# Performance work log

Hardware: AMD Instinct MI355X
Metric: run time of the kernel (lower is better)

Reference implementation:

```python
import jax, jax.numpy as jnp
import numpy as np

DT = 0.01
T, D_IN, D_STATE = 262144, 64, 128

def setup_inputs() -> dict:
    key = jax.random.key(0)
    k1, k2, k3, k4 = jax.random.split(key, 4)
    U = jax.random.normal(k1, (T, D_IN), dtype=jnp.float32)
    A_log = jax.random.normal(k2, (D_STATE,), dtype=jnp.float32) * 0.1 - 1.0
    B = jax.random.normal(k3, (D_STATE, D_IN), dtype=jnp.float32) * 0.1
    C = jax.random.normal(k4, (D_IN, D_STATE), dtype=jnp.float32) * 0.1
    Dm = jnp.zeros((D_IN, D_IN), dtype=jnp.float32)
    h0 = jnp.zeros((D_STATE,), dtype=jnp.float32)
    return {"U": U, "A_log": A_log, "B": B, "C": C, "D": Dm, "h0": h0}

def reference(U, A_log, B, C, D, h0):
    # Discretized diagonal transition: A_disc = exp(A_log * dt)
    A_d = jnp.exp(A_log * DT)  # (d_state,)
    Bu = U @ B.T               # (T, d_state), precompute all input injections
    Du = U @ D.T               # (T, d_input)

    def step(h, bu):
        h_new = A_d * h + bu
        return h_new, h_new

    h_final, H = jax.lax.scan(step, h0, Bu)  # H: (T, d_state)
    Y = H @ C.T + Du                          # (T, d_input)
    return Y, h_final
```

## Files before the change

### kernel.cpp

```cpp
#include <hip/hip_runtime.h>


#define TT   262144
#define DIN  64
#define DS   128
#define DTC  0.01f
#define L    128
#define NG   (TT / L)
#define SEGL 16
#define NSEG (NG / SEGL)

typedef short  s8v  __attribute__((ext_vector_type(8)));
typedef short  s4v  __attribute__((ext_vector_type(4)));
typedef float  f4v  __attribute__((ext_vector_type(4)));

__device__ __forceinline__ unsigned short f2bf(float f) {
    union { __bf16 h; unsigned short u; } cv;
    cv.h = (__bf16)f;
    return cv.u;
}

__device__ __forceinline__ s8v pack8(float4 a, float4 b) {
    union { unsigned short u[8]; s8v v; } r;
    r.u[0] = f2bf(a.x); r.u[1] = f2bf(a.y); r.u[2] = f2bf(a.z); r.u[3] = f2bf(a.w);
    r.u[4] = f2bf(b.x); r.u[5] = f2bf(b.y); r.u[6] = f2bf(b.z); r.u[7] = f2bf(b.w);
    return r.v;
}

__device__ __forceinline__ s4v pack4(float x, float y, float z, float w) {
    union { unsigned short u[4]; s4v v; } r;
    r.u[0] = f2bf(x); r.u[1] = f2bf(y); r.u[2] = f2bf(z); r.u[3] = f2bf(w);
    return r.v;
}

__device__ __forceinline__ int gidx(int NCO, int rtile, int co, int mf) {
    return (((rtile * NCO + co) << 4) + (mf ^ (co & 15))) << 3;
}

__device__ __forceinline__ s8v ldfrag(const unsigned short* S, int NCO,
                                      int rtile, int kt, int q, int m) {
    return *(const s8v*)&S[gidx(NCO, rtile, kt * 4 + q, m)];
}

__device__ __forceinline__ void stage_U(const float* __restrict__ Ug,
                                        unsigned short* __restrict__ sA,
                                        int tid) {
    #pragma unroll
    for (int p = 0; p < 2; ++p) {
        int u  = tid + p * 512;
        int co = u & 7, m = (u >> 3) & 15, mt = u >> 7;
        const float4* gp = (const float4*)(Ug + (mt * 16 + m) * DIN + co * 8);
        *(s8v*)&sA[gidx(8, mt, co, m)] = pack8(gp[0], gp[1]);
    }
}

__device__ __forceinline__ s8v load_bfrag(const float* __restrict__ M,
                                          int row, int k0, int ld) {
    const float4* p = (const float4*)(M + row * ld + k0);
    return pack8(p[0], p[1]);
}

__global__ __launch_bounds__(512) void ssm_k1(
    const float* __restrict__ U, const float* __restrict__ Alog,
    const float* __restrict__ B, float* __restrict__ agg,
    float* __restrict__ segAgg)
{
    __shared__ __align__(16) unsigned short sA[8192];
    const int g    = blockIdx.x;
    const int tid  = threadIdx.x;
    const int lane = tid & 63;
    const int w    = tid >> 6;
    const int q    = lane >> 4, m = lane & 15;
    const int s    = 16 * w + m;

    stage_U(U + (size_t)g * L * DIN, sA, tid);

    s8v Bf[2];
    #pragma unroll
    for (int ks = 0; ks < 2; ++ks)
        Bf[ks] = load_bfrag(B, s, ks * 32 + q * 8, DIN);

    const float cA = Alog[s] * DTC;
    __syncthreads();

    float ainv = __expf(-cA);
    float a16i = __expf(-16.f * cA);
    float wmt  = __expf(cA * (float)(127 - 4 * q));
    float wsum = 0.f;
    #pragma unroll
    for (int mt = 0; mt < 8; ++mt) {
        f4v acc = (f4v){0.f, 0.f, 0.f, 0.f};
        #pragma unroll
        for (int ks = 0; ks < 2; ++ks)
            acc = __builtin_amdgcn_mfma_f32_16x16x32_bf16(
                ldfrag(sA, 8, mt, ks, q, m), Bf[ks], acc, 0, 0, 0);
        float wr = wmt;
        #pragma unroll
        for (int r = 0; r < 4; ++r) {
            wsum = fmaf(wr, acc[r], wsum);
            wr *= ainv;
        }
        wmt *= a16i;
    }
    wsum += __shfl_xor(wsum, 16, 64);
    wsum += __shfl_xor(wsum, 32, 64);

    if (q == 0) {
        agg[(size_t)g * DS + s] = wsum;
        float wgt = __expf(cA * (float)(L * (SEGL - 1 - (g & (SEGL - 1)))));
        atomicAdd(&segAgg[(g >> 4) * DS + s], wsum * wgt);
    }
}

__global__ __launch_bounds__(512, 6) void ssm_k3(
    const float* __restrict__ U, const float* __restrict__ Alog,
    const float* __restrict__ B, const float* __restrict__ C,
    const float* __restrict__ Dm, const float* __restrict__ h0,
    const float* __restrict__ agg, const float* __restrict__ segAgg,
    float* __restrict__ Y, float* __restrict__ hfin)
{
    __shared__ __align__(16) unsigned char smem[49152];
    unsigned short* sA = (unsigned short*)smem;
    unsigned short* sT = (unsigned short*)(smem + 16384);
    float*          sY = (float*)smem;
    __shared__ float sCA[DS];
    __shared__ float sDc[DS];

    const int g    = blockIdx.x;
    const int tid  = threadIdx.x;
    const int lane = tid & 63;
    const int w    = tid >> 6;
    const int q    = lane >> 4, m = lane & 15;

    s8v Bf[2];
    #pragma unroll
    for (int ks = 0; ks < 2; ++ks)
        Bf[ks] = load_bfrag(B, 16 * w + m, ks * 32 + q * 8, DIN);
    const float cA = Alog[16 * w + m] * DTC;

    stage_U(U + (size_t)g * L * DIN, sA, tid);

    if (tid < DS) {
        const float ca  = Alog[tid] * DTC;
        sCA[tid] = ca;
        const float caL = ca * (float)L;
        const float aL  = __expf(caL);
        const int   j   = g & (SEGL - 1);
        const int   gb  = g & ~(SEGL - 1);
        const int   sg  = g >> 4;
        float sc = 0.f;
        if (sg >= 1) sc = segAgg[(sg - 1) * DS + tid];
        if (sg >= 2) sc = fmaf(__expf(caL * 16.f), segAgg[(sg - 2) * DS + tid], sc);
        float c0 = sc * __expf(caL * (float)j);
        float wt = 1.f;
        for (int c = j - 1; c >= 0; --c) {
            c0 = fmaf(wt, agg[(size_t)(gb + c) * DS + tid], c0);
            wt *= aL;
        }
        c0 = fmaf(__expf(caL * (float)g), h0[tid], c0);
        sDc[tid] = __expf(ca) * c0;
        if (g == NG - 1)
            hfin[tid] = fmaf(aL, c0, agg[(size_t)g * DS + tid]);
    }
    __syncthreads();

    {
        float ainv = __expf(-cA);
        float a16i = __expf(-16.f * cA);
        float fmt  = __expf(-cA * (float)(4 * q));
        #pragma unroll
        for (int mt = 0; mt < 8; ++mt) {
            f4v acc = (f4v){0.f, 0.f, 0.f, 0.f};
            #pragma unroll
            for (int ks = 0; ks < 2; ++ks)
                acc = __builtin_amdgcn_mfma_f32_16x16x32_bf16(
                    ldfrag(sA, 8, mt, ks, q, m), Bf[ks], acc, 0, 0, 0);
            float f0 = fmt, f1 = f0 * ainv, f2 = f1 * ainv, f3 = f2 * ainv;
            s4v pk = pack4(acc[0] * f0, acc[1] * f1, acc[2] * f2, acc[3] * f3);
            *(s4v*)&sT[gidx(16, w, mt * 2 + (q >> 1), m) + (q & 1) * 4] = pk;
            fmt *= a16i;
        }
    }
    __syncthreads();

    const int KBmax = w >> 1;
    const int thr   = m + 16 * (w & 1);
    s8v ones, part;
    {
        union { unsigned short u[8]; s8v v; } o, p;
        #pragma unroll
        for (int j = 0; j < 8; ++j) {
            o.u[j] = 0x3F80;
            p.u[j] = (q * 8 + j <= thr) ? 0x3F80 : 0;
        }
        ones = o.v; part = p.v;
    }
    const float tf = (float)(16 * w + m);
    s4v pk[8];
    #pragma unroll
    for (int grp = 0; grp < 2; ++grp) {
        f4v acc[4];
        #pragma unroll
        for (int i = 0; i < 4; ++i) acc[i] = (f4v){0.f, 0.f, 0.f, 0.f};
        for (int kb = 0; kb <= KBmax; ++kb) {
            s8v bfr = (kb < KBmax) ? ones : part;
            #pragma unroll
            for (int msl = 0; msl < 4; ++msl)
                acc[msl] = __builtin_amdgcn_mfma_f32_16x16x32_bf16(
                    ldfrag(sT, 16, grp * 4 + msl, kb, q, m), bfr, acc[msl], 0, 0, 0);
        }
        #pragma unroll
        for (int msl = 0; msl < 4; ++msl) {
            const int ms = grp * 4 + msl;
            const float4 cav = *(const float4*)&sCA[16 * ms + 4 * q];
            const float4 dcv = *(const float4*)&sDc[16 * ms + 4 * q];
            pk[grp * 4 + msl] = pack4(
                __expf(cav.x * tf) * (acc[msl][0] + dcv.x),
                __expf(cav.y * tf) * (acc[msl][1] + dcv.y),
                __expf(cav.z * tf) * (acc[msl][2] + dcv.z),
                __expf(cav.w * tf) * (acc[msl][3] + dcv.w));
        }
    }

    const int mi = w & 3, th = w >> 2;
    float4 craw[4][2], draw[2][2];
    #pragma unroll
    for (int ks = 0; ks < 4; ++ks) {
        const float4* p = (const float4*)(C + (16 * mi + m) * DS + ks * 32 + q * 8);
        craw[ks][0] = p[0]; craw[ks][1] = p[1];
    }
    #pragma unroll
    for (int ks = 0; ks < 2; ++ks) {
        const float4* p = (const float4*)(Dm + (16 * mi + m) * DIN + ks * 32 + q * 8);
        draw[ks][0] = p[0]; draw[ks][1] = p[1];
    }

    __syncthreads();
    #pragma unroll
    for (int ms = 0; ms < 8; ++ms)
        *(s4v*)&sT[gidx(16, w, ms * 2 + (q >> 1), m) + (q & 1) * 4] = pk[ms];
    __syncthreads();

    s8v Cf[4], Df[2];
    #pragma unroll
    for (int ks = 0; ks < 4; ++ks) Cf[ks] = pack8(craw[ks][0], craw[ks][1]);
    #pragma unroll
    for (int ks = 0; ks < 2; ++ks) Df[ks] = pack8(draw[ks][0], draw[ks][1]);

    f4v acc2[4];
    #pragma unroll
    for (int nn = 0; nn < 4; ++nn) {
        const int nt2 = th * 4 + nn;
        f4v a2 = (f4v){0.f, 0.f, 0.f, 0.f};
        #pragma unroll
        for (int ks = 0; ks < 4; ++ks)
            a2 = __builtin_amdgcn_mfma_f32_16x16x32_bf16(
                Cf[ks], ldfrag(sT, 16, nt2, ks, q, m), a2, 0, 0, 0);
        #pragma unroll
        for (int ks = 0; ks < 2; ++ks)
            a2 = __builtin_amdgcn_mfma_f32_16x16x32_bf16(
                Df[ks], ldfrag(sA, 8, nt2, ks, q, m), a2, 0, 0, 0);
        acc2[nn] = a2;
    }
    __syncthreads();

    #pragma unroll
    for (int nn = 0; nn < 4; ++nn) {
        const int t = 16 * (th * 4 + nn) + m;
        *(f4v*)&sY[t * 68 + 16 * mi + 4 * q] = acc2[nn];
    }
    __syncthreads();

    float* Yb = Y + (size_t)g * L * DIN;
    #pragma unroll
    for (int k = 0; k < 4; ++k) {
        const int f   = tid + 512 * k;
        const int row = f >> 4;
        const int col = (f & 15) << 2;
        *(float4*)(Yb + row * 64 + col) = *(const float4*)&sY[row * 68 + col];
    }
}

extern "C" void kernel_launch(void* const* d_in, const int* in_sizes, int n_in,
                              void* d_out, int out_size, void* d_ws, size_t ws_size,
                              hipStream_t stream)
{
    const float* U    = (const float*)d_in[0];
    const float* Alog = (const float*)d_in[1];
    const float* B    = (const float*)d_in[2];
    const float* C    = (const float*)d_in[3];
    const float* Dm   = (const float*)d_in[4];
    const float* h0   = (const float*)d_in[5];

    float* out  = (float*)d_out;
    float* Yp   = out;
    float* hfin = out + (size_t)TT * DIN;

    float* agg    = (float*)d_ws;
    float* segAgg = agg + (size_t)NG * DS;

    hipMemsetAsync(segAgg, 0, (size_t)NSEG * DS * sizeof(float), stream);
    ssm_k1<<<NG, 512, 0, stream>>>(U, Alog, B, agg, segAgg);
    ssm_k3<<<NG, 512, 0, stream>>>(U, Alog, B, C, Dm, h0, agg, segAgg, Yp, hfin);
}
```

Baseline: 191.0 us.

## Remap chunk-aggregate kernel to one wave per chunk with B fragments in registers

The first-pass kernel changes from one 512-thread block per 128-step chunk, where eight waves split the state dimension, to 256-thread blocks where each wave owns a whole chunk. Each wave loops over all eight state tiles and keeps every B fragment in registers. Each wave stages its own U tile into a private LDS slice, so the block-wide barrier goes away. The cost is more registers per wave (16 B fragment vectors) and a serial loop over state tiles inside each wave, which may cut occupancy and add per-wave latency.

```diff
diff --git a/kernel.cpp b/kernel.cpp
--- a/kernel.cpp
+++ b/kernel.cpp
@@ -9,6 +9,7 @@
 #define NG   (TT / L)
 #define SEGL 16
 #define NSEG (NG / SEGL)
+#define WPB  4
 
 typedef short  s8v  __attribute__((ext_vector_type(8)));
 typedef short  s4v  __attribute__((ext_vector_type(4)));
@@ -60,55 +61,66 @@
     return pack8(p[0], p[1]);
 }
 
-__global__ __launch_bounds__(512) void ssm_k1(
+__global__ __launch_bounds__(256) void ssm_k1w(
     const float* __restrict__ U, const float* __restrict__ Alog,
     const float* __restrict__ B, float* __restrict__ agg,
     float* __restrict__ segAgg)
 {
-    __shared__ __align__(16) unsigned short sA[8192];
-    const int g    = blockIdx.x;
+    __shared__ __align__(16) unsigned short sA[WPB][8192];
     const int tid  = threadIdx.x;
     const int lane = tid & 63;
     const int w    = tid >> 6;
+    const int g    = blockIdx.x * WPB + w;
     const int q    = lane >> 4, m = lane & 15;
-    const int s    = 16 * w + m;
-
-    stage_U(U + (size_t)g * L * DIN, sA, tid);
-
-    s8v Bf[2];
-    #pragma unroll
-    for (int ks = 0; ks < 2; ++ks)
-        Bf[ks] = load_bfrag(B, s, ks * 32 + q * 8, DIN);
-
-    const float cA = Alog[s] * DTC;
-    __syncthreads();
-
-    float ainv = __expf(-cA);
-    float a16i = __expf(-16.f * cA);
-    float wmt  = __expf(cA * (float)(127 - 4 * q));
-    float wsum = 0.f;
-    #pragma unroll
-    for (int mt = 0; mt < 8; ++mt) {
-        f4v acc = (f4v){0.f, 0.f, 0.f, 0.f};
+    unsigned short* sAw = &sA[w][0];
+
+    s8v Bf[8][2];
+    #pragma unroll
+    for (int st = 0; st < 8; ++st)
         #pragma unroll
         for (int ks = 0; ks < 2; ++ks)
-            acc = __builtin_amdgcn_mfma_f32_16x16x32_bf16(
-                ldfrag(sA, 8, mt, ks, q, m), Bf[ks], acc, 0, 0, 0);
-        float wr = wmt;
-        #pragma unroll
-        for (int r = 0; r < 4; ++r) {
-            wsum = fmaf(wr, acc[r], wsum);
-            wr *= ainv;
-        }
-        wmt *= a16i;
-    }
-    wsum += __shfl_xor(wsum, 16, 64);
-    wsum += __shfl_xor(wsum, 32, 64);
-
-    if (q == 0) {
-        agg[(size_t)g * DS + s] = wsum;
-        float wgt = __expf(cA * (float)(L * (SEGL - 1 - (g & (SEGL - 1)))));
-        atomicAdd(&segAgg[(g >> 4) * DS + s], wsum * wgt);
+            Bf[st][ks] = load_bfrag(B, 16 * st + m, ks * 32 + q * 8, DIN);
+
+    const float* Ug = U + (size_t)g * L * DIN;
+    #pragma unroll
+    for (int p = 0; p < 16; ++p) {
+        int u  = lane + p * 64;
+        int co = u & 7, mf = (u >> 3) & 15, mt = u >> 7;
+        const float4* gp = (const float4*)(Ug + (mt * 16 + mf) * DIN + co * 8);
+        *(s8v*)&sAw[gidx(8, mt, co, mf)] = pack8(gp[0], gp[1]);
+    }
+
+    const int sgi = (g >> 4) * DS;
+    const float wexp = (float)(L * (SEGL - 1 - (g & (SEGL - 1))));
+    #pragma unroll
+    for (int st = 0; st < 8; ++st) {
+        const int   s    = 16 * st + m;
+        const float cA   = Alog[s] * DTC;
+        const float ainv = __expf(-cA);
+        const float a16i = __expf(-16.f * cA);
+        float wmt  = __expf(cA * (float)(127 - 4 * q));
+        float wsum = 0.f;
+        #pragma unroll
+        for (int mt = 0; mt < 8; ++mt) {
+            f4v acc = (f4v){0.f, 0.f, 0.f, 0.f};
+            #pragma unroll
+            for (int ks = 0; ks < 2; ++ks)
+                acc = __builtin_amdgcn_mfma_f32_16x16x32_bf16(
+                    ldfrag(sAw, 8, mt, ks, q, m), Bf[st][ks], acc, 0, 0, 0);
+            float wr = wmt;
+            #pragma unroll
+            for (int r = 0; r < 4; ++r) {
+                wsum = fmaf(wr, acc[r], wsum);
+                wr *= ainv;
+            }
+            wmt *= a16i;
+        }
+        wsum += __shfl_xor(wsum, 16, 64);
+        wsum += __shfl_xor(wsum, 32, 64);
+        if (q == 0) {
+            agg[(size_t)g * DS + s] = wsum;
+            atomicAdd(&segAgg[sgi + s], wsum * __expf(cA * wexp));
+        }
     }
 }
 
@@ -300,6 +312,6 @@
     float* segAgg = agg + (size_t)NG * DS;
 
     hipMemsetAsync(segAgg, 0, (size_t)NSEG * DS * sizeof(float), stream);
-    ssm_k1<<<NG, 512, 0, stream>>>(U, Alog, B, agg, segAgg);
+    ssm_k1w<<<NG / WPB, 64 * WPB, 0, stream>>>(U, Alog, B, agg, segAgg);
     ssm_k3<<<NG, 512, 0, stream>>>(U, Alog, B, C, Dm, h0, agg, segAgg, Yp, hfin);
 }
```

New measurement: 198.1 us. 3.8% more time.
